# Performance work log

Measured on AMD Instinct MI355X. Metric: run time of the kernel, lower is better.

## Reference

```python
import jax, jax.numpy as jnp
import numpy as np

B, S = 16, 128
V_W, V_C = 32000, 128
E, CD, H, L, CLS = 300, 50, 100, 20, 3
EPS = 1e-8


def _lstm(x, Wih, Whh, b):
    # x: (B, T, I); PyTorch gate order i, f, g, o
    Bb, Hh = x.shape[0], Whh.shape[1]
    def step(carry, xt):
        h, c = carry
        z = xt @ Wih.T + h @ Whh.T + b
        i, f, g, o = jnp.split(z, 4, axis=-1)
        c = jax.nn.sigmoid(f) * c + jax.nn.sigmoid(i) * jnp.tanh(g)
        h = jax.nn.sigmoid(o) * jnp.tanh(c)
        return (h, c), h
    h0 = jnp.zeros((Bb, Hh), x.dtype)
    (hT, _), hs = jax.lax.scan(step, (h0, h0), x.swapaxes(0, 1))
    return hs.swapaxes(0, 1), hT  # (B,T,H), (B,H)


def _bilstm_out(x, Wf, Uf, bf, Wb, Ub, bb):
    of, _ = _lstm(x, Wf, Uf, bf)
    ob, _ = _lstm(x[:, ::-1], Wb, Ub, bb)
    return of, ob[:, ::-1]


def _agg_last(x, Wf, Uf, bf, Wb, Ub, bb):
    _, hf = _lstm(x, Wf, Uf, bf)
    _, hb = _lstm(x[:, ::-1], Wb, Ub, bb)
    return jnp.concatenate([hf, hb], -1)  # (B, 2H)


def _mp_match(v1, v2, w):
    # cos(w_l * v1, w_l * v2) without materializing (B,S,H,L)
    if v2.ndim == 2:
        v2 = v2[:, None, :]
    ws = w * w  # (L,H)
    num = jnp.einsum('bsh,lh->bsl', v1 * v2, ws)
    n1 = jnp.sqrt(jnp.einsum('bsh,lh->bsl', v1 * v1, ws))
    n2 = jnp.sqrt(jnp.einsum('bsh,lh->bsl', v2 * v2, ws))
    return num / jnp.maximum(n1 * n2, EPS)


def _cos_att(v1, v2):
    a = jnp.einsum('bph,bqh->bpq', v1, v2)
    n1 = jnp.linalg.norm(v1, axis=2)[:, :, None]
    n2 = jnp.linalg.norm(v2, axis=2)[:, None, :]
    return a / jnp.maximum(n1 * n2, EPS)


def _branch(p_fw, p_bw, h_fw, h_bw, w1, w2, w3, w4, w5, w6):
    mp_full_fw = _mp_match(p_fw, h_fw[:, -1, :], w1)
    mp_full_bw = _mp_match(p_bw, h_bw[:, 0, :], w2)
    mh_full_fw = _mp_match(h_fw, p_fw[:, -1, :], w1)
    mh_full_bw = _mp_match(h_bw, p_bw[:, 0, :], w2)

    def att_feats(pv, hv):
        att = _cos_att(pv, hv)  # (B,P,Q)
        mean_h = jnp.einsum('bpq,bqh->bph', att, hv) / jnp.maximum(att.sum(2, keepdims=True), EPS)
        mean_p = jnp.einsum('bpq,bph->bqh', att, pv) / jnp.maximum(att.sum(1)[:, :, None], EPS)
        max_h = jnp.max(hv[:, None, :, :] * att[..., None], axis=2)  # (B,P,H)
        max_p = jnp.max(pv[:, :, None, :] * att[..., None], axis=1)  # (B,Q,H)
        return mean_h, mean_p, max_h, max_p

    mean_h_fw, mean_p_fw, max_h_fw, max_p_fw = att_feats(p_fw, h_fw)
    mean_h_bw, mean_p_bw, max_h_bw, max_p_bw = att_feats(p_bw, h_bw)

    mp_mean_fw = _mp_match(p_fw, mean_h_fw, w3)
    mp_mean_bw = _mp_match(p_bw, mean_h_bw, w4)
    mh_mean_fw = _mp_match(h_fw, mean_p_fw, w3)
    mh_mean_bw = _mp_match(h_bw, mean_p_bw, w4)
    mp_max_fw = _mp_match(p_fw, max_h_fw, w5)
    mp_max_bw = _mp_match(p_bw, max_h_bw, w6)
    mh_max_fw = _mp_match(h_fw, max_p_fw, w5)
    mh_max_bw = _mp_match(h_bw, max_p_bw, w6)

    mv_p = jnp.concatenate([mp_full_fw, mp_mean_fw, mp_max_fw, mp_full_bw, mp_mean_bw, mp_max_bw], 2)
    mv_h = jnp.concatenate([mh_full_fw, mh_mean_fw, mh_max_fw, mh_full_bw, mh_mean_bw, mh_max_bw], 2)
    return mv_p, mv_h  # (B,S,6L)


def _highway(x, lw, lb, gw, gb):
    hlin = jax.nn.relu(x @ lw.T + lb)
    t = jax.nn.sigmoid(x @ gw.T + gb)
    return t * hlin + (1.0 - t) * x


def setup_inputs():
    key = jax.random.key(0)
    keys = iter(jax.random.split(key, 80))
    def rn(*shape):
        return jax.random.normal(next(keys), shape, jnp.float32) * 0.1
    d = {}
    d['p_ids'] = jax.random.randint(next(keys), (B, S), 0, V_W)
    d['h_ids'] = jax.random.randint(next(keys), (B, S), 0, V_W)
    d['cp_ids'] = jax.random.randint(next(keys), (B, S), 0, V_C)
    d['ch_ids'] = jax.random.randint(next(keys), (B, S), 0, V_C)
    d['word_emb'] = rn(V_W, E)
    d['char_emb'] = rn(V_C, CD)
    for pref, inp in (('ctx', E), ('chr', CD), ('agg', 6 * L)):
        for dd in ('f', 'b'):
            d[pref + '_Wih_' + dd] = rn(4 * H, inp)
            d[pref + '_Whh_' + dd] = rn(4 * H, H)
            d[pref + '_b_' + dd] = jnp.zeros((4 * H,), jnp.float32)
    for i in range(1, 7):
        d['mp_w%d' % i] = rn(L, H)
    d['char_w1'] = rn(L, H)
    d['char_w2'] = rn(L, H)
    d['hw_lin_w'] = rn(4 * H, 4 * H)
    d['hw_lin_b'] = jnp.zeros((4 * H,), jnp.float32)
    d['hw_gate_w'] = rn(4 * H, 4 * H)
    d['hw_gate_b'] = jnp.zeros((4 * H,), jnp.float32)
    d['fc1_w'] = rn(2 * H, 8 * H)
    d['fc1_b'] = jnp.zeros((2 * H,), jnp.float32)
    d['fc2_w'] = rn(CLS, 2 * H)
    d['fc2_b'] = jnp.zeros((CLS,), jnp.float32)
    return d


def reference(p_ids, h_ids, cp_ids, ch_ids, word_emb, char_emb,
              ctx_Wih_f, ctx_Whh_f, ctx_b_f, ctx_Wih_b, ctx_Whh_b, ctx_b_b,
              chr_Wih_f, chr_Whh_f, chr_b_f, chr_Wih_b, chr_Whh_b, chr_b_b,
              agg_Wih_f, agg_Whh_f, agg_b_f, agg_Wih_b, agg_Whh_b, agg_b_b,
              mp_w1, mp_w2, mp_w3, mp_w4, mp_w5, mp_w6, char_w1, char_w2,
              hw_lin_w, hw_lin_b, hw_gate_w, hw_gate_b, fc1_w, fc1_b, fc2_w, fc2_b):
    agg = (agg_Wih_f, agg_Whh_f, agg_b_f, agg_Wih_b, agg_Whh_b, agg_b_b)
    ctx = (ctx_Wih_f, ctx_Whh_f, ctx_b_f, ctx_Wih_b, ctx_Whh_b, ctx_b_b)
    chr_ = (chr_Wih_f, chr_Whh_f, chr_b_f, chr_Wih_b, chr_Whh_b, chr_b_b)

    # word path
    p_fw, p_bw = _bilstm_out(word_emb[p_ids], *ctx)
    h_fw, h_bw = _bilstm_out(word_emb[h_ids], *ctx)
    mv_p, mv_h = _branch(p_fw, p_bw, h_fw, h_bw, mp_w1, mp_w2, mp_w3, mp_w4, mp_w5, mp_w6)
    wx = jnp.concatenate([_agg_last(mv_p, *agg), _agg_last(mv_h, *agg)], -1)  # (B,4H)

    # char path (code applies mp_w3..6 to char branch; requires char_hidden == hidden)
    cp_fw, cp_bw = _bilstm_out(char_emb[cp_ids], *chr_)
    ch_fw, ch_bw = _bilstm_out(char_emb[ch_ids], *chr_)
    cmv_p, cmv_h = _branch(cp_fw, cp_bw, ch_fw, ch_bw, char_w1, char_w2, mp_w3, mp_w4, mp_w5, mp_w6)
    cx = jnp.concatenate([_agg_last(cmv_p, *agg), _agg_last(cmv_h, *agg)], -1)  # (B,4H)

    wx = _highway(wx, hw_lin_w, hw_lin_b, hw_gate_w, hw_gate_b)
    cx = _highway(cx, hw_lin_w, hw_lin_b, hw_gate_w, hw_gate_b)
    x = jnp.tanh(jnp.concatenate([wx, cx], -1) @ fc1_w.T + fc1_b)
    return x @ fc2_w.T + fc2_b  # (B, CLS)
```

## Files before the change

kernel.cpp:

```cpp
#include <hip/hip_runtime.h>


#define Bz 16
#define Sz 128
#define Hz 100
#define Gz 400
#define NT 25
#define EPSV 1e-8f

#define XIN_CH  ((long)Sz * Bz * Gz)
#define HOUT_CH ((long)Bz * Sz * Hz)
#define MV_CH   ((long)Bz * Sz * 120)

typedef __attribute__((ext_vector_type(4))) float floatx4;
typedef __attribute__((ext_vector_type(8))) __bf16 bf16x8;

union FragU { bf16x8 v; unsigned u[4]; unsigned short s[8]; };

__device__ __forceinline__ float bf2f(unsigned short h) {
  unsigned u = ((unsigned)h) << 16;
  return __builtin_bit_cast(float, u);
}
__device__ __forceinline__ unsigned short f2bf(float x) {
  unsigned u = __builtin_bit_cast(unsigned, x);
  u = u + 0x7FFFu + ((u >> 16) & 1u);
  return (unsigned short)(u >> 16);
}
__device__ __forceinline__ float rcpf(float x) { return __builtin_amdgcn_rcpf(x); }
__device__ __forceinline__ float sigf(float x) { return rcpf(1.0f + __expf(-x)); }
__device__ __forceinline__ float tanh_fast(float x) {
  return 1.0f - 2.0f * rcpf(__expf(2.0f * x) + 1.0f);
}

__device__ __forceinline__ void barrier_lds_only() {
  __asm__ __volatile__("s_waitcnt lgkmcnt(0)\ns_barrier" ::: "memory");
}

#define MFMA(a, b, c) __builtin_amdgcn_mfma_f32_16x16x32_bf16((a), (b), (c), 0, 0, 0)

__device__ __forceinline__ int pv_chain(int grp) { return (grp < 2 ? 0 : 4) + (grp & 1); }

struct CvtDesc { const float* src; unsigned short* dst; int K; int KP; };
struct Cvt6 { CvtDesc d[6]; };

__global__ __launch_bounds__(64) void k_cvt(Cvt6 C) {
  int bx = blockIdx.x;
  int m = bx / Gz;
  int p = bx % Gz;
  CvtDesc d = C.d[m];
  int orig = (p & 3) * Hz + (p >> 2);
  const float* src = d.src + (long)orig * d.K;
  unsigned short* dst = d.dst + (long)p * d.KP;
  for (int k = threadIdx.x; k < d.KP; k += 64)
    dst[k] = (k < d.K) ? f2bf(src[k]) : 0;
}

struct ProjChain {
  const int* ids;
  const float* emb;
  const float* src;
  const unsigned short* W16;
  const float* bias;
  float* out;
  int rev;
  int K;
  int nch;
};
struct Proj8 { ProjChain c[8]; };

#define PPS 328

__global__ __launch_bounds__(256) void k_proj(Proj8 P) {
  __shared__ __align__(16) unsigned short phi[16 * PPS];
  __shared__ __align__(16) unsigned short plo[16 * PPS];

  int bx = blockIdx.x;
  int c = bx >> 7;
  int t = bx & 127;
  const ProjChain ch = P.c[c];
  const int K = ch.K;
  const int KP = ch.nch * 32;
  int tp = ch.rev ? (Sz - 1 - t) : t;
  int tid = threadIdx.x;

  for (int i = tid; i < 16 * KP; i += 256) {
    int b = i / KP, k = i % KP;
    float v = 0.f;
    if (k < K) {
      const float* row = ch.ids ? (ch.emb + (long)ch.ids[b * Sz + tp] * K)
                                : (ch.src + ((long)b * Sz + tp) * K);
      v = row[k];
    }
    unsigned u = __builtin_bit_cast(unsigned, v);
    phi[b * PPS + k] = (unsigned short)(u >> 16);
    float hi = __builtin_bit_cast(float, u & 0xFFFF0000u);
    unsigned ul = __builtin_bit_cast(unsigned, v - hi);
    plo[b * PPS + k] = (unsigned short)(ul >> 16);
  }
  __syncthreads();

  int w = tid >> 6, lane = tid & 63;
  int nl = lane & 15, qd = lane >> 4;
  floatx4 acc[7];
#pragma unroll
  for (int i = 0; i < 7; ++i) acc[i] = floatx4{0.f, 0.f, 0.f, 0.f};

  const unsigned short* wbase[7];
#pragma unroll
  for (int i = 0; i < 7; ++i) {
    int nt = w + 4 * i;
    wbase[i] = (nt < NT) ? (ch.W16 + (long)(nt * 16 + nl) * KP) : ch.W16;
  }

  for (int cc = 0; cc < ch.nch; ++cc) {
    FragU bhi, blo;
    bhi.v = *(const bf16x8*)&phi[nl * PPS + cc * 32 + qd * 8];
    blo.v = *(const bf16x8*)&plo[nl * PPS + cc * 32 + qd * 8];
    int ko = cc * 32 + qd * 8;
#pragma unroll
    for (int i = 0; i < 7; ++i) {
      if (w + 4 * i < NT) {
        FragU whi;
        whi.v = *(const bf16x8*)(wbase[i] + ko);
        acc[i] = MFMA(whi.v, bhi.v, acc[i]);
        acc[i] = MFMA(whi.v, blo.v, acc[i]);
      }
    }
  }
#pragma unroll
  for (int i = 0; i < 7; ++i) {
    int nt = w + 4 * i;
    if (nt < NT) {
#pragma unroll
      for (int r = 0; r < 4; ++r) {
        int p = nt * 16 + qd * 4 + r;
        acc[i][r] += ch.bias[(p & 3) * Hz + (p >> 2)];
      }
      *(floatx4*)(ch.out + ((long)t * Bz + nl) * Gz + nt * 16 + qd * 4) = acc[i];
    }
  }
}

struct LstmChain {
  const float* xin;
  const float* Whh;
  float* hout;
  int rev;
  int store_all;
};
struct Lstm8 { LstmChain c[8]; };

#define NW 8
#define TPW 4
#define NCH 7
#define HPR 232

__global__ __launch_bounds__(512, 2) void k_lstm(Lstm8 P) {
  __shared__ __align__(16) unsigned short hpk[2][Bz * HPR];
  __shared__ float hfp[2][Bz * Hz];

  const LstmChain ch = P.c[blockIdx.x];
  const int tid = threadIdx.x;
  const int w = tid >> 6;
  const int lane = tid & 63;
  const int nl = lane & 15;
  const int qd = lane >> 4;

  for (int i = tid; i < 2 * Bz * HPR / 2; i += 512) ((unsigned*)hpk)[i] = 0;
  __syncthreads();

  FragU wa[TPW][NCH];
#pragma unroll
  for (int i = 0; i < TPW; ++i) {
    int tile = i * NW + w;
    if (tile < NT) {
      int pA = tile * 16 + nl;
      const float* wr = ch.Whh + (long)((pA & 3) * Hz + (pA >> 2)) * Hz;
#pragma unroll
      for (int cc = 0; cc < NCH; ++cc) {
#pragma unroll
        for (int j = 0; j < 8; ++j) {
          int k = cc * 16 + qd * 4 + (j >> 1);
          wa[i][cc].s[j] = f2bf((k < Hz) ? wr[k] : 0.f);
        }
      }
    }
  }

  floatx4 xc[TPW], xn[TPW];
  float cstate[TPW];
#pragma unroll
  for (int i = 0; i < TPW; ++i) {
    cstate[i] = 0.f;
    xc[i] = floatx4{0.f, 0.f, 0.f, 0.f};
    if (i * NW + w < NT)
      xc[i] = *(const floatx4*)(ch.xin + (long)nl * Gz + (i * NW + w) * 16 + qd * 4);
  }

  for (int t = 0; t < Sz; ++t) {
    if (ch.store_all && t > 0) {
      int pb = (t - 1) & 1;
      int sprev = ch.rev ? (Sz - t) : (t - 1);
#pragma unroll
      for (int it = 0; it < 4; ++it) {
        int idx = tid + it * 512;
        if (idx < Bz * Hz)
          ch.hout[((long)(idx / Hz) * Sz + sprev) * Hz + (idx % Hz)] = hfp[pb][idx];
      }
    }
    if (t + 1 < Sz) {
      const float* xp = ch.xin + (long)(t + 1) * Bz * Gz + (long)nl * Gz;
#pragma unroll
      for (int i = 0; i < TPW; ++i)
        if (i * NW + w < NT)
          xn[i] = *(const floatx4*)(xp + (i * NW + w) * 16 + qd * 4);
    }
    const int rp = t & 1;
    floatx4 acc[TPW];
#pragma unroll
    for (int i = 0; i < TPW; ++i) acc[i] = xc[i];
#pragma unroll
    for (int cc = 0; cc < NCH; ++cc) {
      FragU bh;
      bh.v = *(const bf16x8*)(&hpk[rp][nl * HPR + cc * 32 + qd * 8]);
#pragma unroll
      for (int i = 0; i < TPW; ++i)
        if (i * NW + w < NT) acc[i] = MFMA(wa[i][cc].v, bh.v, acc[i]);
    }
    const int wp = rp ^ 1;
    const bool keep = ch.store_all || (t == Sz - 1);
#pragma unroll
    for (int i = 0; i < TPW; ++i) {
      int tile = i * NW + w;
      if (tile < NT) {
        float cn = sigf(acc[i][1]) * cstate[i] + sigf(acc[i][0]) * tanh_fast(acc[i][2]);
        float h = sigf(acc[i][3]) * tanh_fast(cn);
        cstate[i] = cn;
        int hd = tile * 4 + qd;
        unsigned u = __builtin_bit_cast(unsigned, h);
        float hi = __builtin_bit_cast(float, u & 0xFFFF0000u);
        unsigned ul = __builtin_bit_cast(unsigned, h - hi);
        *(unsigned*)(&hpk[wp][nl * HPR + 2 * hd]) = (u >> 16) | (ul & 0xFFFF0000u);
        if (keep) hfp[t & 1][nl * Hz + hd] = h;
      }
    }
    barrier_lds_only();
#pragma unroll
    for (int i = 0; i < TPW; ++i) xc[i] = xn[i];
  }
  {
    int pb = (Sz - 1) & 1;
    int slast = ch.rev ? 0 : (Sz - 1);
#pragma unroll
    for (int it = 0; it < 4; ++it) {
      int idx = tid + it * 512;
      if (idx < Bz * Hz)
        ch.hout[((long)(idx / Hz) * Sz + slast) * Hz + (idx % Hz)] = hfp[pb][idx];
    }
  }
}

#define PVS2 102
#define FS 104

struct BranchArgs {
  const float* houtA;
  float* mv;
  const float* w_full[4];
  const float* w3; const float* w4; const float* w5; const float* w6;
};

__global__ __launch_bounds__(512, 1) void k_branch(BranchArgs G) {
  __shared__ float pvs[128 * PVS2];
  __shared__ float hvs[128 * PVS2 + 32];
  __shared__ float wl[60 * PVS2];
  __shared__ float attw[8 * 128];
  __shared__ float fmean[8 * FS];
  __shared__ float fmax[8 * FS];
  __shared__ float nrmp[128], nrmh[128];

  int bx = blockIdx.x;
  int grp = bx >> 6;
  int b = (bx >> 2) & 15;
  int side = (bx >> 1) & 1;
  int rh = bx & 1;
  int fw = !(grp & 1);
  int word = grp < 2;
  int pc = pv_chain(grp);
  const float* PV = G.houtA + (long)pc * HOUT_CH + (long)b * Sz * Hz;
  const float* HV = G.houtA + (long)(pc + 2) * HOUT_CH + (long)b * Sz * Hz;
  int tid = threadIdx.x;
  int w = tid >> 6, lane = tid & 63;

  for (int i = tid; i < 128 * Hz; i += 512) {
    int r = i / Hz, c = i % Hz;
    pvs[r * PVS2 + c] = PV[r * Hz + c];
    hvs[r * PVS2 + c] = HV[r * Hz + c];
  }
  {
    const float* wm = fw ? G.w3 : G.w4;
    const float* wx = fw ? G.w5 : G.w6;
    const float* wf = G.w_full[grp];
    for (int i = tid; i < 60 * Hz; i += 512) {
      int row = i / Hz, c = i % Hz;
      const float* src = (row < 20) ? wf : (row < 40 ? wm : wx);
      int rr = (row < 20) ? row : (row < 40 ? row - 20 : row - 40);
      wl[row * PVS2 + c] = src[rr * Hz + c];
    }
  }
  __syncthreads();
  if (tid < 256) {
    const float* base = (tid < 128) ? pvs : hvs;
    int r = tid & 127;
    float s = 0.f;
    for (int j = 0; j < Hz; ++j) { float v = base[r * PVS2 + j]; s += v * v; }
    if (tid < 128) nrmp[r] = sqrtf(s); else nrmh[r] = sqrtf(s);
  }
  __syncthreads();

  const float* A  = side ? hvs : pvs;
  const float* B  = side ? pvs : hvs;
  const float* nA = side ? nrmh : nrmp;
  const float* nB = side ? nrmp : nrmh;
  int bcrow = fw ? (Sz - 1) : 0;
  float* mvout = G.mv + (long)((word ? 0 : 2) + side) * MV_CH + (long)b * Sz * 120;
  int off = fw ? 0 : 60;
  int type = lane / 20;
  const float* wrow = wl + lane * PVS2;
  float* myatt = attw + w * 128;
  float* myfm = fmean + w * FS;
  float* myfx = fmax + w * FS;

  for (int task = w; task < 64; task += 8) {
    int r = rh * 64 + task;
    const float* ar = A + r * PVS2;
    float d0 = 0.f, d1 = 0.f;
    const float* b0 = B + lane * PVS2;
    const float* b1 = B + (lane + 64) * PVS2;
    for (int j = 0; j < Hz; j += 2) {
      float2 a2 = *(const float2*)(ar + j);
      float2 p2 = *(const float2*)(b0 + j);
      float2 q2 = *(const float2*)(b1 + j);
      d0 += a2.x * p2.x + a2.y * p2.y;
      d1 += a2.x * q2.x + a2.y * q2.y;
    }
    float at0 = d0 * rcpf(fmaxf(nA[r] * nB[lane], EPSV));
    float at1 = d1 * rcpf(fmaxf(nA[r] * nB[lane + 64], EPSV));
    myatt[lane] = at0;
    myatt[lane + 64] = at1;
    float s = at0 + at1;
#pragma unroll
    for (int m = 1; m < 64; m <<= 1) s += __shfl_xor(s, m);
    float inv = rcpf(fmaxf(s, EPSV));
    float m0 = 0.f, m1 = 0.f, x0 = -1e30f, x1 = -1e30f;
    const float* bj0 = B + lane;
    const float* bj1 = B + lane + 64;
    for (int q = 0; q < 128; ++q) {
      float aq = myatt[q];
      float v0 = bj0[q * PVS2];
      float v1 = bj1[q * PVS2];
      m0 += aq * v0; x0 = fmaxf(x0, aq * v0);
      m1 += aq * v1; x1 = fmaxf(x1, aq * v1);
    }
    myfm[lane] = m0 * inv;
    myfx[lane] = x0;
    if (lane < Hz - 64) { myfm[lane + 64] = m1 * inv; myfx[lane + 64] = x1; }
    if (lane < 60) {
      const float* v2p = (type == 0) ? (B + bcrow * PVS2)
                       : (type == 1) ? myfm : myfx;
      float num = 0.f, n1 = 0.f, n2 = 0.f;
      for (int j = 0; j < Hz; j += 2) {
        float2 w2 = *(const float2*)(wrow + j);
        float2 a2 = *(const float2*)(ar + j);
        float2 c2 = *(const float2*)(v2p + j);
        float ws0 = w2.x * w2.x, ws1 = w2.y * w2.y;
        num += ws0 * a2.x * c2.x + ws1 * a2.y * c2.y;
        n1  += ws0 * a2.x * a2.x + ws1 * a2.y * a2.y;
        n2  += ws0 * c2.x * c2.x + ws1 * c2.y * c2.y;
      }
      mvout[r * 120 + off + lane] = num * rcpf(fmaxf(sqrtf(n1) * sqrtf(n2), EPSV));
    }
  }
}

__global__ __launch_bounds__(1024) void k_head(const float* houtB,
                                               const float* lw, const float* lb,
                                               const float* gw, const float* gb,
                                               const float* f1w, const float* f1b,
                                               const float* f2w, const float* f2b,
                                               float* out) {
  int b = blockIdx.x;
  __shared__ float xr[800];
  __shared__ float hwv[800];
  __shared__ float f1[200];
  int tid = threadIdx.x;
  if (tid < 800) {
    int seq = tid / Gz;
    int i = tid % Gz;
    int seg = i / Hz, j = i % Hz;
    int chain = seq * 4 + seg;
    int s_sel = (seg & 1) ? 0 : (Sz - 1);
    xr[tid] = houtB[((long)chain * Bz + b) * Sz * Hz + (long)s_sel * Hz + j];
  }
  __syncthreads();
  if (tid < 800) {
    int seq = tid / Gz;
    int o = tid % Gz;
    const float* xs = xr + seq * Gz;
    const float* lwr = lw + (long)o * Gz;
    const float* gwr = gw + (long)o * Gz;
    float al = 0.f, ag = 0.f;
#pragma unroll 4
    for (int k = 0; k < Gz; ++k) {
      float x = xs[k];
      al += x * lwr[k];
      ag += x * gwr[k];
    }
    al += lb[o];
    ag += gb[o];
    float hlin = fmaxf(al, 0.f);
    float tg = sigf(ag);
    hwv[tid] = tg * hlin + (1.f - tg) * xs[o];
  }
  __syncthreads();
  if (tid < 200) {
    const float* wr = f1w + (long)tid * 800;
    float acc = f1b[tid];
#pragma unroll 4
    for (int k = 0; k < 800; ++k) acc += hwv[k] * wr[k];
    f1[tid] = tanh_fast(acc);
  }
  __syncthreads();
  if (tid < 3) {
    const float* wr = f2w + tid * 200;
    float acc = f2b[tid];
    for (int k = 0; k < 200; ++k) acc += f1[k] * wr[k];
    out[b * 3 + tid] = acc;
  }
}

extern "C" void kernel_launch(void* const* d_in, const int* in_sizes, int n_in,
                              void* d_out, int out_size, void* d_ws, size_t ws_size,
                              hipStream_t stream) {
  (void)in_sizes; (void)n_in; (void)out_size;

  const int* p_ids  = (const int*)d_in[0];
  const int* h_ids  = (const int*)d_in[1];
  const int* cp_ids = (const int*)d_in[2];
  const int* ch_ids = (const int*)d_in[3];
  const float* word_emb = (const float*)d_in[4];
  const float* char_emb = (const float*)d_in[5];
  const float* ctx_Wih_f = (const float*)d_in[6];
  const float* ctx_Whh_f = (const float*)d_in[7];
  const float* ctx_b_f   = (const float*)d_in[8];
  const float* ctx_Wih_b = (const float*)d_in[9];
  const float* ctx_Whh_b = (const float*)d_in[10];
  const float* ctx_b_b   = (const float*)d_in[11];
  const float* chr_Wih_f = (const float*)d_in[12];
  const float* chr_Whh_f = (const float*)d_in[13];
  const float* chr_b_f   = (const float*)d_in[14];
  const float* chr_Wih_b = (const float*)d_in[15];
  const float* chr_Whh_b = (const float*)d_in[16];
  const float* chr_b_b   = (const float*)d_in[17];
  const float* agg_Wih_f = (const float*)d_in[18];
  const float* agg_Whh_f = (const float*)d_in[19];
  const float* agg_b_f   = (const float*)d_in[20];
  const float* agg_Wih_b = (const float*)d_in[21];
  const float* agg_Whh_b = (const float*)d_in[22];
  const float* agg_b_b   = (const float*)d_in[23];
  const float* mp_w1 = (const float*)d_in[24];
  const float* mp_w2 = (const float*)d_in[25];
  const float* mp_w3 = (const float*)d_in[26];
  const float* mp_w4 = (const float*)d_in[27];
  const float* mp_w5 = (const float*)d_in[28];
  const float* mp_w6 = (const float*)d_in[29];
  const float* char_w1 = (const float*)d_in[30];
  const float* char_w2 = (const float*)d_in[31];
  const float* hw_lin_w  = (const float*)d_in[32];
  const float* hw_lin_b  = (const float*)d_in[33];
  const float* hw_gate_w = (const float*)d_in[34];
  const float* hw_gate_b = (const float*)d_in[35];
  const float* fc1_w = (const float*)d_in[36];
  const float* fc1_b = (const float*)d_in[37];
  const float* fc2_w = (const float*)d_in[38];
  const float* fc2_b = (const float*)d_in[39];

  float* ws = (float*)d_ws;
  float* XIN    = ws;
  float* HOUT_A = XIN + 8 * XIN_CH;
  float* HOUT_B = HOUT_A + 8 * HOUT_CH;
  float* MV     = HOUT_B + 8 * HOUT_CH;
  unsigned short* WC = (unsigned short*)(MV + 4 * MV_CH);
  unsigned short* W_ctx_f = WC;
  unsigned short* W_ctx_b = W_ctx_f + (long)Gz * 320;
  unsigned short* W_chr_f = W_ctx_b + (long)Gz * 320;
  unsigned short* W_chr_b = W_chr_f + (long)Gz * 64;
  unsigned short* W_agg_f = W_chr_b + (long)Gz * 64;
  unsigned short* W_agg_b = W_agg_f + (long)Gz * 128;
  size_t needed = (size_t)((char*)(W_agg_b + (long)Gz * 128) - (char*)ws);
  if (ws_size < needed) return;

  {
    Cvt6 cv{};
    cv.d[0] = {ctx_Wih_f, W_ctx_f, 300, 320};
    cv.d[1] = {ctx_Wih_b, W_ctx_b, 300, 320};
    cv.d[2] = {chr_Wih_f, W_chr_f, 50, 64};
    cv.d[3] = {chr_Wih_b, W_chr_b, 50, 64};
    cv.d[4] = {agg_Wih_f, W_agg_f, 120, 128};
    cv.d[5] = {agg_Wih_b, W_agg_b, 120, 128};
    k_cvt<<<6 * Gz, 64, 0, stream>>>(cv);
  }
  {
    Proj8 pc{};
    const int* idv[8] = {p_ids, p_ids, h_ids, h_ids, cp_ids, cp_ids, ch_ids, ch_ids};
    for (int c = 0; c < 8; ++c) {
      int word = c < 4;
      pc.c[c].ids = idv[c];
      pc.c[c].emb = word ? word_emb : char_emb;
      pc.c[c].src = nullptr;
      pc.c[c].W16  = word ? ((c & 1) ? W_ctx_b : W_ctx_f) : ((c & 1) ? W_chr_b : W_chr_f);
      pc.c[c].bias = word ? ((c & 1) ? ctx_b_b : ctx_b_f) : ((c & 1) ? chr_b_b : chr_b_f);
      pc.c[c].out = XIN + c * XIN_CH;
      pc.c[c].rev = c & 1;
      pc.c[c].K = word ? 300 : 50;
      pc.c[c].nch = word ? 10 : 2;
    }
    k_proj<<<8 * Sz, 256, 0, stream>>>(pc);
  }
  {
    Lstm8 la{};
    for (int c = 0; c < 8; ++c) {
      la.c[c].xin = XIN + c * XIN_CH;
      la.c[c].Whh = (c < 4) ? ((c & 1) ? ctx_Whh_b : ctx_Whh_f)
                            : ((c & 1) ? chr_Whh_b : chr_Whh_f);
      la.c[c].hout = HOUT_A + c * HOUT_CH;
      la.c[c].rev = c & 1;
      la.c[c].store_all = 1;
    }
    k_lstm<<<8, 512, 0, stream>>>(la);
  }
  {
    BranchArgs g{};
    g.houtA = HOUT_A; g.mv = MV;
    g.w_full[0] = mp_w1; g.w_full[1] = mp_w2; g.w_full[2] = char_w1; g.w_full[3] = char_w2;
    g.w3 = mp_w3; g.w4 = mp_w4; g.w5 = mp_w5; g.w6 = mp_w6;
    k_branch<<<256, 512, 0, stream>>>(g);
  }
  {
    Proj8 pa{};
    for (int c = 0; c < 8; ++c) {
      pa.c[c].ids = nullptr; pa.c[c].emb = nullptr;
      pa.c[c].src = MV + (c >> 1) * MV_CH;
      pa.c[c].W16 = (c & 1) ? W_agg_b : W_agg_f;
      pa.c[c].bias = (c & 1) ? agg_b_b : agg_b_f;
      pa.c[c].out = XIN + c * XIN_CH;
      pa.c[c].rev = c & 1;
      pa.c[c].K = 120;
      pa.c[c].nch = 4;
    }
    k_proj<<<8 * Sz, 256, 0, stream>>>(pa);
  }
  {
    Lstm8 la{};
    for (int c = 0; c < 8; ++c) {
      la.c[c].xin = XIN + c * XIN_CH;
      la.c[c].Whh = (c & 1) ? agg_Whh_b : agg_Whh_f;
      la.c[c].hout = HOUT_B + c * HOUT_CH;
      la.c[c].rev = c & 1;
      la.c[c].store_all = 0;
    }
    k_lstm<<<8, 512, 0, stream>>>(la);
  }
  k_head<<<Bz, 1024, 0, stream>>>(HOUT_B, hw_lin_w, hw_lin_b, hw_gate_w, hw_gate_b,
                                  fc1_w, fc1_b, fc2_w, fc2_b, (float*)d_out);
}
```

Baseline: 746.8 us.

## Widen LSTM recurrence to 16 waves with split hi/lo bf16 hidden-state MFMAs

The recurrent LSTM kernel now runs with 1024 threads (16 waves, 2 tiles per wave) instead of 512, which shortens the per-step serial MFMA chain in each wave. The hidden state is stored as separate hi and lo bf16 buffers, and the K dimension is packed with 32 real values per chunk (4 chunks instead of 7 interleaved ones), costing two MFMAs per chunk. Global-store address arithmetic for the hidden outputs is also hoisted out of the time loop. Costs are a larger per-step barrier across 16 waves and more register pressure under the 1024-thread launch bound.

```diff
diff --git a/kernel.cpp b/kernel.cpp
--- a/kernel.cpp
+++ b/kernel.cpp
@@ -150,13 +150,14 @@
 };
 struct Lstm8 { LstmChain c[8]; };
 
-#define NW 8
-#define TPW 4
-#define NCH 7
-#define HPR 232
-
-__global__ __launch_bounds__(512, 2) void k_lstm(Lstm8 P) {
-  __shared__ __align__(16) unsigned short hpk[2][Bz * HPR];
+#define NW 16
+#define TPW 2
+#define NCH 4
+#define HPR 160
+
+__global__ __launch_bounds__(1024, 4) void k_lstm(Lstm8 P) {
+  __shared__ __align__(16) unsigned short hhi[2][Bz * HPR];
+  __shared__ __align__(16) unsigned short hlo[2][Bz * HPR];
   __shared__ float hfp[2][Bz * Hz];
 
   const LstmChain ch = P.c[blockIdx.x];
@@ -166,7 +167,10 @@
   const int nl = lane & 15;
   const int qd = lane >> 4;
 
-  for (int i = tid; i < 2 * Bz * HPR / 2; i += 512) ((unsigned*)hpk)[i] = 0;
+  for (int i = tid; i < Bz * HPR; i += 1024) {
+    ((unsigned*)hhi)[i] = 0;
+    ((unsigned*)hlo)[i] = 0;
+  }
   __syncthreads();
 
   FragU wa[TPW][NCH];
@@ -180,11 +184,21 @@
       for (int cc = 0; cc < NCH; ++cc) {
 #pragma unroll
         for (int j = 0; j < 8; ++j) {
-          int k = cc * 16 + qd * 4 + (j >> 1);
+          int k = cc * 32 + qd * 8 + j;
           wa[i][cc].s[j] = f2bf((k < Hz) ? wr[k] : 0.f);
         }
       }
     }
+  }
+
+  long hbase[2]; int hok[2]; int hidx[2];
+#pragma unroll
+  for (int it = 0; it < 2; ++it) {
+    int idx = tid + it * 1024;
+    hok[it] = idx < Bz * Hz;
+    int bq = idx / Hz, rq = idx - bq * Hz;
+    hbase[it] = (long)bq * Sz * Hz + rq;
+    hidx[it] = idx;
   }
 
   floatx4 xc[TPW], xn[TPW];
@@ -202,11 +216,9 @@
       int pb = (t - 1) & 1;
       int sprev = ch.rev ? (Sz - t) : (t - 1);
 #pragma unroll
-      for (int it = 0; it < 4; ++it) {
-        int idx = tid + it * 512;
-        if (idx < Bz * Hz)
-          ch.hout[((long)(idx / Hz) * Sz + sprev) * Hz + (idx % Hz)] = hfp[pb][idx];
-      }
+      for (int it = 0; it < 2; ++it)
+        if (hok[it])
+          ch.hout[hbase[it] + (long)sprev * Hz] = hfp[pb][hidx[it]];
     }
     if (t + 1 < Sz) {
       const float* xp = ch.xin + (long)(t + 1) * Bz * Gz + (long)nl * Gz;
@@ -221,11 +233,15 @@
     for (int i = 0; i < TPW; ++i) acc[i] = xc[i];
 #pragma unroll
     for (int cc = 0; cc < NCH; ++cc) {
-      FragU bh;
-      bh.v = *(const bf16x8*)(&hpk[rp][nl * HPR + cc * 32 + qd * 8]);
+      FragU bhi, blo;
+      bhi.v = *(const bf16x8*)(&hhi[rp][nl * HPR + cc * 32 + qd * 8]);
+      blo.v = *(const bf16x8*)(&hlo[rp][nl * HPR + cc * 32 + qd * 8]);
 #pragma unroll
       for (int i = 0; i < TPW; ++i)
-        if (i * NW + w < NT) acc[i] = MFMA(wa[i][cc].v, bh.v, acc[i]);
+        if (i * NW + w < NT) {
+          acc[i] = MFMA(wa[i][cc].v, bhi.v, acc[i]);
+          acc[i] = MFMA(wa[i][cc].v, blo.v, acc[i]);
+        }
     }
     const int wp = rp ^ 1;
     const bool keep = ch.store_all || (t == Sz - 1);
@@ -240,7 +256,8 @@
         unsigned u = __builtin_bit_cast(unsigned, h);
         float hi = __builtin_bit_cast(float, u & 0xFFFF0000u);
         unsigned ul = __builtin_bit_cast(unsigned, h - hi);
-        *(unsigned*)(&hpk[wp][nl * HPR + 2 * hd]) = (u >> 16) | (ul & 0xFFFF0000u);
+        hhi[wp][nl * HPR + hd] = (unsigned short)(u >> 16);
+        hlo[wp][nl * HPR + hd] = (unsigned short)(ul >> 16);
         if (keep) hfp[t & 1][nl * Hz + hd] = h;
       }
     }
@@ -252,11 +269,9 @@
     int pb = (Sz - 1) & 1;
     int slast = ch.rev ? 0 : (Sz - 1);
 #pragma unroll
-    for (int it = 0; it < 4; ++it) {
-      int idx = tid + it * 512;
-      if (idx < Bz * Hz)
-        ch.hout[((long)(idx / Hz) * Sz + slast) * Hz + (idx % Hz)] = hfp[pb][idx];
-    }
+    for (int it = 0; it < 2; ++it)
+      if (hok[it])
+        ch.hout[hbase[it] + (long)slast * Hz] = hfp[pb][hidx[it]];
   }
 }
 
@@ -537,7 +552,7 @@
       la.c[c].rev = c & 1;
       la.c[c].store_all = 1;
     }
-    k_lstm<<<8, 512, 0, stream>>>(la);
+    k_lstm<<<8, 1024, 0, stream>>>(la);
   }
   {
     BranchArgs g{};
@@ -569,7 +584,7 @@
       la.c[c].rev = c & 1;
       la.c[c].store_all = 0;
     }
-    k_lstm<<<8, 512, 0, stream>>>(la);
+    k_lstm<<<8, 1024, 0, stream>>>(la);
   }
   k_head<<<Bz, 1024, 0, stream>>>(HOUT_B, hw_lin_w, hw_lin_b, hw_gate_w, hw_gate_b,
                                   fc1_w, fc1_b, fc2_w, fc2_b, (float*)d_out);
```

New measurement: 683.3 us. 1.09x faster.
